# Kernel optimization log

Hardware: AMD Instinct MI355X
Metric: run time of the kernel (lower is better)

The kernel has to match this reference:

```python
import jax, jax.numpy as jnp
import numpy as np

B, T, P, V, D, DINO, H, L = 32, 40, 256, 4096, 256, 384, 4, 2
HD = D // H          # head dim 64
DFF = 4 * D          # 1024
EPS = 1e-5


def setup_inputs() -> dict:
    key = jax.random.key(0)
    ks = iter(jax.random.split(key, 40))
    rn = lambda shape, s=0.02: jax.random.normal(next(ks), shape, jnp.float32) * s
    return dict(
        patches=jax.random.normal(next(ks), (B, P, DINO), jnp.float32),
        tokens=jax.random.randint(next(ks), (B, T), 0, V, jnp.int32),
        tok_emb=rn((V, D)),
        pos_emb=rn((1, T, D)),
        qkv_w=rn((L, 3 * D, D)), qkv_b=jnp.zeros((L, 3 * D), jnp.float32),
        out_w=rn((L, D, D)), out_b=jnp.zeros((L, D), jnp.float32),
        ln1_s=jnp.ones((L, D), jnp.float32), ln1_b=jnp.zeros((L, D), jnp.float32),
        w1=rn((L, DFF, D)), b1=jnp.zeros((L, DFF), jnp.float32),
        w2=rn((L, D, DFF)), b2=jnp.zeros((L, D), jnp.float32),
        ln2_s=jnp.ones((L, D), jnp.float32), ln2_b=jnp.zeros((L, D), jnp.float32),
        fus_w1=rn((D, DINO + D)), fus_b1=jnp.zeros((D,), jnp.float32),
        fus_w2=rn((D, D)), fus_b2=jnp.zeros((D,), jnp.float32),
        cls_w=rn((V, D)), cls_b=jnp.zeros((V,), jnp.float32),
    )


def _ln(x, s, b):
    m = jnp.mean(x, -1, keepdims=True)
    v = jnp.var(x, -1, keepdims=True)
    return (x - m) * jax.lax.rsqrt(v + EPS) * s + b


def _token_encoder(tokens, tok_emb, pos_emb, qkv_w, qkv_b, out_w, out_b,
                   ln1_s, ln1_b, w1, b1, w2, b2, ln2_s, ln2_b):
    # Causal full-sequence pass: output at position t equals re-running the
    # unmasked encoder on tokens[:, :t+1] and taking the last position.
    x = tok_emb[tokens] + pos_emb[:, :tokens.shape[1], :]   # [B,T,D]
    causal = jnp.triu(jnp.full((T, T), -1e9, jnp.float32), 1)  # [T,T]
    for l in range(L):  # fixed small layer count
        qkv = x @ qkv_w[l].T + qkv_b[l]                     # [B,T,3D]
        q, k, v = jnp.split(qkv, 3, axis=-1)
        q = q.reshape(B, T, H, HD).transpose(0, 2, 1, 3)    # [B,H,T,hd]
        k = k.reshape(B, T, H, HD).transpose(0, 2, 1, 3)
        v = v.reshape(B, T, H, HD).transpose(0, 2, 1, 3)
        scores = jnp.einsum('bhqd,bhkd->bhqk', q, k) / np.sqrt(HD).astype(np.float32)
        attn = jax.nn.softmax(scores + causal, axis=-1)
        ctx = jnp.einsum('bhqk,bhkd->bhqd', attn, v)        # [B,H,T,hd]
        ctx = ctx.transpose(0, 2, 1, 3).reshape(B, T, D)
        x = _ln(x + ctx @ out_w[l].T + out_b[l], ln1_s[l], ln1_b[l])
        h = jax.nn.relu(x @ w1[l].T + b1[l]) @ w2[l].T + b2[l]
        x = _ln(x + h, ln2_s[l], ln2_b[l])
    return x  # [B,T,D]


def reference(patches, tokens, tok_emb, pos_emb, qkv_w, qkv_b, out_w, out_b,
              ln1_s, ln1_b, w1, b1, w2, b2, ln2_s, ln2_b,
              fus_w1, fus_b1, fus_w2, fus_b2, cls_w, cls_b):
    enc = _token_encoder(tokens, tok_emb, pos_emb, qkv_w, qkv_b, out_w, out_b,
                         ln1_s, ln1_b, w1, b1, w2, b2, ln2_s, ln2_b)  # [B,T,D]
    # context for step 0 is zeros; step t>0 uses encoder output at position t-1
    ctx = jnp.concatenate([jnp.zeros((B, 1, D), enc.dtype), enc[:, :-1]], axis=1)  # [B,T,D]
    # fusion MLP: split the concat-linear into a patch part and a context part
    wp, wc = fus_w1[:, :DINO], fus_w1[:, DINO:]
    pproj = patches @ wp.T                                  # [B,P,D]
    cproj = ctx @ wc.T + fus_b1                             # [B,T,D]
    h = jax.nn.gelu(pproj[:, None, :, :] + cproj[:, :, None, :], approximate=False)  # [B,T,P,D]
    fused = h @ fus_w2.T + fus_b2                           # [B,T,P,D]
    # sigmoid+gather of the 4096-way logits == gather classifier rows, dot, sigmoid
    w_sel = cls_w[tokens]                                   # [B,T,D]
    b_sel = cls_b[tokens]                                   # [B,T]
    logits = jnp.einsum('btpd,btd->btp', fused, w_sel) + b_sel[:, :, None]
    probs = jax.nn.sigmoid(logits)                          # [B,T,P]
    return probs.transpose(0, 2, 1)                         # [B,P,T] == [B,256,40]
```

## Files before the change

kernel.cpp:

```cpp
#include <hip/hip_runtime.h>
#include <hip/hip_bf16.h>

#define B_ 32
#define T_ 40
#define P_ 256
#define V_ 4096
#define D_ 256
#define DINO_ 384
#define H_ 4
#define L_ 2
#define HD_ 64
#define DFF_ 1024
#define EPS_ 1e-5f

typedef __bf16 bf16;
typedef __bf16 bf16x8 __attribute__((ext_vector_type(8)));
typedef float f32x4 __attribute__((ext_vector_type(4)));

#define OFF_QKV 0
#define OFF_OUTW 393216
#define OFF_W1 524288
#define OFF_W2 1048576
#define OFF_FUS 1572864
#define WB_TOTAL 1736704
#define CONV_BLOCKS 848

__device__ __forceinline__ bf16x8 cvt8(const float* p) {
  float4 f0 = *(const float4*)p;
  float4 f1 = *(const float4*)(p + 4);
  bf16x8 v;
  v[0] = (bf16)f0.x; v[1] = (bf16)f0.y; v[2] = (bf16)f0.z; v[3] = (bf16)f0.w;
  v[4] = (bf16)f1.x; v[5] = (bf16)f1.y; v[6] = (bf16)f1.z; v[7] = (bf16)f1.w;
  return v;
}

__global__ __launch_bounds__(256) void prep_k(
    const int* __restrict__ tokens, const float* __restrict__ tok_emb,
    const float* __restrict__ pos_emb, float* __restrict__ x,
    const float* __restrict__ fus_w2, bf16* __restrict__ w2Tb,
    const float* __restrict__ qkv_w, const float* __restrict__ out_w,
    const float* __restrict__ w1, const float* __restrict__ w2,
    const float* __restrict__ fus_w1, bf16* __restrict__ wb) {
  __shared__ float tile[32][33];
  int bi = blockIdx.x;
  int tid = threadIdx.x;
  if (bi < B_ * T_) {
    int t = bi % T_;
    x[bi * D_ + tid] = tok_emb[tokens[bi] * D_ + tid] + pos_emb[t * D_ + tid];
  } else if (bi < B_ * T_ + 64) {
    int tt = bi - B_ * T_;
    int bx = (tt & 7) * 32, by = (tt >> 3) * 32;
    int tx = tid & 31, ty = tid >> 5;
#pragma unroll
    for (int i = 0; i < 32; i += 8) tile[ty + i][tx] = fus_w2[(by + ty + i) * D_ + bx + tx];
    __syncthreads();
#pragma unroll
    for (int i = 0; i < 32; i += 8)
      w2Tb[(bx + ty + i) * D_ + by + tx] = (bf16)tile[tx][ty + i];
  } else {
    long f = (long)(bi - B_ * T_ - 64) * 2048 + tid * 8;
    const float* src;
    long off;
    if (f < OFF_OUTW)      { src = qkv_w;  off = f - OFF_QKV; }
    else if (f < OFF_W1)   { src = out_w;  off = f - OFF_OUTW; }
    else if (f < OFF_W2)   { src = w1;     off = f - OFF_W1; }
    else if (f < OFF_FUS)  { src = w2;     off = f - OFF_W2; }
    else                   { src = fus_w1; off = f - OFF_FUS; }
    *(bf16x8*)&wb[f] = cvt8(src + off);
  }
}

__global__ __launch_bounds__(256) void gemm_k(
    const float* __restrict__ A, const bf16* __restrict__ W,
    const float* __restrict__ bias, float* __restrict__ out,
    int K, int lda, int ldw, int ldc, int relu) {
  __shared__ bf16 As[32 * 72];
  __shared__ bf16 Ws[32 * 72];
  const int tid = threadIdx.x;
  const int lane = tid & 63;
  const int wv = tid >> 6;
  const int mi = wv & 1, ni = wv >> 1;
  const int col = lane & 15;
  const int quad = lane >> 4;
  const int bn = blockIdx.x * 32;
  const int bm = blockIdx.y * 32;
  const int srow = tid >> 3;
  const int kc = (tid & 7) * 8;
  const float* Ap = A + (long)(bm + srow) * lda;
  const bf16* Wp = W + (long)(bn + srow) * ldw;

  f32x4 acc = {0.f, 0.f, 0.f, 0.f};
  for (int kk = 0; kk < K; kk += 64) {
    *(bf16x8*)&As[srow * 72 + kc] = cvt8(Ap + kk + kc);
    *(bf16x8*)&Ws[srow * 72 + kc] = *(const bf16x8*)(Wp + kk + kc);
    __syncthreads();
#pragma unroll
    for (int ki = 0; ki < 2; ++ki) {
      bf16x8 afr = *(const bf16x8*)&As[(mi * 16 + col) * 72 + ki * 32 + quad * 8];
      bf16x8 bfr = *(const bf16x8*)&Ws[(ni * 16 + col) * 72 + ki * 32 + quad * 8];
      acc = __builtin_amdgcn_mfma_f32_16x16x32_bf16(afr, bfr, acc, 0, 0, 0);
    }
    __syncthreads();
  }
  const int n = bn + ni * 16 + col;
  float bv = bias ? bias[n] : 0.0f;
#pragma unroll
  for (int r = 0; r < 4; ++r) {
    int m = bm + mi * 16 + quad * 4 + r;
    float val = acc[r] + bv;
    if (relu) val = fmaxf(val, 0.0f);
    out[(long)m * ldc + n] = val;
  }
}

__global__ __launch_bounds__(256) void fuse3_k(
    const float* __restrict__ patches, const float* __restrict__ xbuf,
    const float* __restrict__ cls_w, const bf16* __restrict__ fusb,
    const bf16* __restrict__ w2Tb, const float* __restrict__ fus_b1,
    const int* __restrict__ tokens, float* __restrict__ pprojT,
    float* __restrict__ cw) {
  __shared__ bf16 As[32 * 72];
  __shared__ bf16 Ws[32 * 72];
  const int tid = threadIdx.x;
  const int lane = tid & 63;
  const int wv = tid >> 6;
  const int mi = wv & 1, ni = wv >> 1;
  const int col = lane & 15;
  const int quad = lane >> 4;
  const int bn = blockIdx.x * 32;
  const int y = blockIdx.y;
  const int srow = tid >> 3;
  const int kc = (tid & 7) * 8;

  int job, bm;
  if (y < 256) { job = 0; bm = y * 32; }
  else if (y < 296) { job = 1; bm = (y - 256) * 32; }
  else { job = 2; bm = (y - 296) * 32; }
  const int gm = bm + srow;

  const float* Ap;
  const bf16* Wp;
  int K;
  bool zeroA = false;
  if (job == 0) {
    Ap = patches + (long)gm * DINO_;
    Wp = fusb + (long)(bn + srow) * 640;
    K = DINO_;
  } else if (job == 1) {
    int t = gm % T_;
    zeroA = (t == 0);
    Ap = xbuf + (long)(zeroA ? gm : gm - 1) * D_;
    Wp = fusb + 384 + (long)(bn + srow) * 640;
    K = D_;
  } else {
    Ap = cls_w + (long)tokens[gm] * D_;
    Wp = w2Tb + (long)(bn + srow) * D_;
    K = D_;
  }

  f32x4 acc = {0.f, 0.f, 0.f, 0.f};
  bf16x8 z8 = {};
  for (int kk = 0; kk < K; kk += 64) {
    bf16x8 av = zeroA ? z8 : cvt8(Ap + kk + kc);
    *(bf16x8*)&As[srow * 72 + kc] = av;
    *(bf16x8*)&Ws[srow * 72 + kc] = *(const bf16x8*)(Wp + kk + kc);
    __syncthreads();
#pragma unroll
    for (int ki = 0; ki < 2; ++ki) {
      bf16x8 afr = *(const bf16x8*)&As[(mi * 16 + col) * 72 + ki * 32 + quad * 8];
      bf16x8 bfr = *(const bf16x8*)&Ws[(ni * 16 + col) * 72 + ki * 32 + quad * 8];
      acc = __builtin_amdgcn_mfma_f32_16x16x32_bf16(afr, bfr, acc, 0, 0, 0);
    }
    __syncthreads();
  }
  const int n = bn + ni * 16 + col;
  if (job == 0) {
#pragma unroll
    for (int r = 0; r < 4; ++r) {
      int m = bm + mi * 16 + quad * 4 + r;
      int b = m >> 8, p = m & 255;
      pprojT[(long)b * (D_ * P_) + (long)n * P_ + p] = acc[r];
    }
  } else if (job == 1) {
    float bv = fus_b1[n];
#pragma unroll
    for (int r = 0; r < 4; ++r) {
      int m = bm + mi * 16 + quad * 4 + r;
      cw[(long)m * (2 * D_) + n * 2] = acc[r] + bv;
    }
  } else {
#pragma unroll
    for (int r = 0; r < 4; ++r) {
      int m = bm + mi * 16 + quad * 4 + r;
      cw[(long)m * (2 * D_) + n * 2 + 1] = acc[r];
    }
  }
}

__global__ __launch_bounds__(256) void attn_k(const float* __restrict__ qkv,
                                              float* __restrict__ ctx) {
  __shared__ float q[T_][HD_ + 1];
  __shared__ float k[T_][HD_ + 1];
  __shared__ float v[T_][HD_ + 1];
  __shared__ float s[T_][T_ + 1];
  int h = blockIdx.x, b = blockIdx.y;
  int tid = threadIdx.x;
  for (int idx = tid; idx < T_ * HD_; idx += 256) {
    int t = idx >> 6, d = idx & 63;
    long base = (long)(b * T_ + t) * (3 * D_) + h * HD_ + d;
    q[t][d] = qkv[base];
    k[t][d] = qkv[base + D_];
    v[t][d] = qkv[base + 2 * D_];
  }
  __syncthreads();
  for (int idx = tid; idx < T_ * T_; idx += 256) {
    int i = idx / T_, j = idx - i * T_;
    if (j <= i) {
      float acc = 0.f;
#pragma unroll
      for (int d = 0; d < HD_; ++d) acc += q[i][d] * k[j][d];
      s[i][j] = acc * 0.125f;
    }
  }
  __syncthreads();
  if (tid < T_) {
    int i = tid;
    float mx = -1e30f;
    for (int j = 0; j <= i; ++j) mx = fmaxf(mx, s[i][j]);
    float sum = 0.f;
    for (int j = 0; j <= i; ++j) {
      float e = __expf(s[i][j] - mx);
      s[i][j] = e;
      sum += e;
    }
    float inv = 1.0f / sum;
    for (int j = 0; j <= i; ++j) s[i][j] *= inv;
  }
  __syncthreads();
  for (int idx = tid; idx < T_ * HD_; idx += 256) {
    int i = idx >> 6, d = idx & 63;
    float acc = 0.f;
    for (int j = 0; j <= i; ++j) acc += s[i][j] * v[j][d];
    ctx[(long)(b * T_ + i) * D_ + h * HD_ + d] = acc;
  }
}

__global__ __launch_bounds__(256) void ln_k(float* __restrict__ x, const float* __restrict__ y,
                                            const float* __restrict__ g,
                                            const float* __restrict__ be) {
  __shared__ float red[4];
  int m = blockIdx.x, d = threadIdx.x;
  int lane = d & 63, wv = d >> 6;
  float val = x[m * D_ + d] + y[m * D_ + d];
  float sv = val;
#pragma unroll
  for (int mk = 1; mk < 64; mk <<= 1) sv += __shfl_xor(sv, mk);
  if (lane == 0) red[wv] = sv;
  __syncthreads();
  float mean = (red[0] + red[1] + red[2] + red[3]) * (1.0f / D_);
  __syncthreads();
  float c = val - mean;
  float s2 = c * c;
#pragma unroll
  for (int mk = 1; mk < 64; mk <<= 1) s2 += __shfl_xor(s2, mk);
  if (lane == 0) red[wv] = s2;
  __syncthreads();
  float var = (red[0] + red[1] + red[2] + red[3]) * (1.0f / D_);
  x[m * D_ + d] = c * rsqrtf(var + EPS_) * g[d] + be[d];
}

__global__ __launch_bounds__(256) void final_k(const float* __restrict__ pprojT,
                                               const float* __restrict__ cw,
                                               const int* __restrict__ tokens,
                                               const float* __restrict__ cls_w,
                                               const float* __restrict__ cls_b,
                                               const float* __restrict__ fus_b2,
                                               float* __restrict__ out) {
  int lane = threadIdx.x & 63, wv = threadIdx.x >> 6;
  int p = blockIdx.x * 64 + lane;
  int t = blockIdx.y * 4 + wv;
  int b = blockIdx.z;
  int m = b * T_ + t;
  int tok = tokens[m];
  const float* cr = cls_w + (long)tok * D_;
  float bacc = 0.f;
#pragma unroll
  for (int i = 0; i < 4; ++i) bacc += cr[lane + i * 64] * fus_b2[lane + i * 64];
#pragma unroll
  for (int mk = 1; mk < 64; mk <<= 1) bacc += __shfl_xor(bacc, mk);
  float beff = bacc + cls_b[tok];

  const float* ppb = pprojT + (long)b * (D_ * P_);
  const float* cwt = cw + (long)m * (D_ * 2);
  float acc = 0.f;
#pragma unroll 8
  for (int e = 0; e < D_; ++e) {
    float pp = ppb[e * P_ + p];
    float2 c = *(const float2*)&cwt[e * 2];
    float x = pp + c.x;
    float x2 = x * x;
    float u = x * fmaf(-0.1029432f, x2, -2.3022083f);
    float ex = __builtin_amdgcn_exp2f(u);
    float r = __builtin_amdgcn_rcpf(1.0f + ex);
    acc = fmaf(x * r, c.y, acc);
  }
  float logit = acc + beff;
  float es = __builtin_amdgcn_exp2f(-1.4426950408889634f * logit);
  out[(long)(b * P_ + p) * T_ + t] = __builtin_amdgcn_rcpf(1.0f + es);
}

extern "C" void kernel_launch(void* const* d_in, const int* in_sizes, int n_in, void* d_out,
                              int out_size, void* d_ws, size_t ws_size, hipStream_t stream) {
  const float* patches = (const float*)d_in[0];
  const int* tokens = (const int*)d_in[1];
  const float* tok_emb = (const float*)d_in[2];
  const float* pos_emb = (const float*)d_in[3];
  const float* qkv_w = (const float*)d_in[4];
  const float* qkv_b = (const float*)d_in[5];
  const float* out_w = (const float*)d_in[6];
  const float* out_b = (const float*)d_in[7];
  const float* ln1_s = (const float*)d_in[8];
  const float* ln1_b = (const float*)d_in[9];
  const float* w1 = (const float*)d_in[10];
  const float* b1 = (const float*)d_in[11];
  const float* w2 = (const float*)d_in[12];
  const float* b2 = (const float*)d_in[13];
  const float* ln2_s = (const float*)d_in[14];
  const float* ln2_b = (const float*)d_in[15];
  const float* fus_w1 = (const float*)d_in[16];
  const float* fus_b1 = (const float*)d_in[17];
  const float* fus_w2 = (const float*)d_in[18];
  const float* fus_b2 = (const float*)d_in[19];
  const float* cls_w = (const float*)d_in[20];
  const float* cls_b = (const float*)d_in[21];
  float* out = (float*)d_out;

  float* xbuf = (float*)d_ws;
  float* qkvbuf = xbuf + B_ * T_ * D_;
  float* tmp = qkvbuf + B_ * T_ * 3 * D_;
  float* hbuf = tmp + B_ * T_ * D_;
  float* pprojT = hbuf + B_ * T_ * DFF_;
  float* cwbuf = pprojT + (long)B_ * D_ * P_;
  bf16* wb = (bf16*)(cwbuf + B_ * T_ * D_ * 2);
  bf16* w2Tb = wb + WB_TOTAL;

  const int MT = B_ * T_;

  prep_k<<<MT + 64 + CONV_BLOCKS, 256, 0, stream>>>(
      tokens, tok_emb, pos_emb, xbuf, fus_w2, w2Tb, qkv_w, out_w, w1, w2, fus_w1, wb);

  for (int l = 0; l < L_; ++l) {
    gemm_k<<<dim3(24, 40), 256, 0, stream>>>(
        xbuf, wb + OFF_QKV + (long)l * 3 * D_ * D_, qkv_b + l * 3 * D_, qkvbuf,
        D_, D_, D_, 3 * D_, 0);
    attn_k<<<dim3(H_, B_), 256, 0, stream>>>(qkvbuf, hbuf);
    gemm_k<<<dim3(8, 40), 256, 0, stream>>>(
        hbuf, wb + OFF_OUTW + (long)l * D_ * D_, out_b + l * D_, tmp,
        D_, D_, D_, D_, 0);
    ln_k<<<MT, D_, 0, stream>>>(xbuf, tmp, ln1_s + l * D_, ln1_b + l * D_);
    gemm_k<<<dim3(32, 40), 256, 0, stream>>>(
        xbuf, wb + OFF_W1 + (long)l * DFF_ * D_, b1 + l * DFF_, hbuf,
        D_, D_, D_, DFF_, 1);
    gemm_k<<<dim3(8, 40), 256, 0, stream>>>(
        hbuf, wb + OFF_W2 + (long)l * D_ * DFF_, b2 + l * D_, tmp,
        DFF_, DFF_, DFF_, D_, 0);
    ln_k<<<MT, D_, 0, stream>>>(xbuf, tmp, ln2_s + l * D_, ln2_b + l * D_);
  }

  fuse3_k<<<dim3(8, 336), 256, 0, stream>>>(patches, xbuf, cls_w, wb + OFF_FUS, w2Tb,
                                            fus_b1, tokens, pprojT, cwbuf);

  final_k<<<dim3(4, 10, 32), 256, 0, stream>>>(pprojT, cwbuf, tokens, cls_w, cls_b,
                                               fus_b2, out);
}
```

Measured before the change: 269.8 us.

## Fuse residual into GEMMs, bf16 FFN hidden, split attention, LDS-cache final context

```diff
diff --git a/kernel.cpp b/kernel.cpp
--- a/kernel.cpp
+++ b/kernel.cpp
@@ -24,6 +24,7 @@
 #define OFF_FUS 1572864
 #define WB_TOTAL 1736704
 #define CONV_BLOCKS 848
+#define PAT_BLOCKS 1536
 
 __device__ __forceinline__ bf16x8 cvt8(const float* p) {
   float4 f0 = *(const float4*)p;
@@ -40,7 +41,8 @@
     const float* __restrict__ fus_w2, bf16* __restrict__ w2Tb,
     const float* __restrict__ qkv_w, const float* __restrict__ out_w,
     const float* __restrict__ w1, const float* __restrict__ w2,
-    const float* __restrict__ fus_w1, bf16* __restrict__ wb) {
+    const float* __restrict__ fus_w1, bf16* __restrict__ wb,
+    const float* __restrict__ patches, bf16* __restrict__ patb) {
   __shared__ float tile[32][33];
   int bi = blockIdx.x;
   int tid = threadIdx.x;
@@ -57,7 +59,7 @@
 #pragma unroll
     for (int i = 0; i < 32; i += 8)
       w2Tb[(bx + ty + i) * D_ + by + tx] = (bf16)tile[tx][ty + i];
-  } else {
+  } else if (bi < B_ * T_ + 64 + CONV_BLOCKS) {
     long f = (long)(bi - B_ * T_ - 64) * 2048 + tid * 8;
     const float* src;
     long off;
@@ -67,32 +69,37 @@
     else if (f < OFF_FUS)  { src = w2;     off = f - OFF_W2; }
     else                   { src = fus_w1; off = f - OFF_FUS; }
     *(bf16x8*)&wb[f] = cvt8(src + off);
-  }
-}
-
+  } else {
+    long f = (long)(bi - B_ * T_ - 64 - CONV_BLOCKS) * 2048 + tid * 8;
+    *(bf16x8*)&patb[f] = cvt8(patches + f);
+  }
+}
+
+template <int ABF16, int OBF16, int RELU, int RESID>
 __global__ __launch_bounds__(256) void gemm_k(
-    const float* __restrict__ A, const bf16* __restrict__ W,
-    const float* __restrict__ bias, float* __restrict__ out,
-    int K, int lda, int ldw, int ldc, int relu) {
+    const void* __restrict__ Av, const bf16* __restrict__ W,
+    const float* __restrict__ bias, const float* __restrict__ resid,
+    void* __restrict__ outv, int K, int lda, int ldw, int ldc) {
   __shared__ bf16 As[32 * 72];
   __shared__ bf16 Ws[32 * 72];
   const int tid = threadIdx.x;
   const int lane = tid & 63;
   const int wv = tid >> 6;
   const int mi = wv & 1, ni = wv >> 1;
-  const int col = lane & 15;
-  const int quad = lane >> 4;
-  const int bn = blockIdx.x * 32;
-  const int bm = blockIdx.y * 32;
-  const int srow = tid >> 3;
-  const int kc = (tid & 7) * 8;
-  const float* Ap = A + (long)(bm + srow) * lda;
-  const bf16* Wp = W + (long)(bn + srow) * ldw;
+  const int col = lane & 15, quad = lane >> 4;
+  const int bn = blockIdx.x * 32, bm = blockIdx.y * 32;
+  const int srow = tid >> 3, kc = (tid & 7) * 8;
+  const float* Af = (const float*)Av;
+  const bf16* Ab = (const bf16*)Av;
+  const bf16* Wp = W + (long)(bn + srow) * ldw + kc;
 
   f32x4 acc = {0.f, 0.f, 0.f, 0.f};
   for (int kk = 0; kk < K; kk += 64) {
-    *(bf16x8*)&As[srow * 72 + kc] = cvt8(Ap + kk + kc);
-    *(bf16x8*)&Ws[srow * 72 + kc] = *(const bf16x8*)(Wp + kk + kc);
+    if (ABF16)
+      *(bf16x8*)&As[srow * 72 + kc] = *(const bf16x8*)(Ab + (long)(bm + srow) * lda + kk + kc);
+    else
+      *(bf16x8*)&As[srow * 72 + kc] = cvt8(Af + (long)(bm + srow) * lda + kk + kc);
+    *(bf16x8*)&Ws[srow * 72 + kc] = *(const bf16x8*)(Wp + kk);
     __syncthreads();
 #pragma unroll
     for (int ki = 0; ki < 2; ++ki) {
@@ -108,13 +115,91 @@
   for (int r = 0; r < 4; ++r) {
     int m = bm + mi * 16 + quad * 4 + r;
     float val = acc[r] + bv;
-    if (relu) val = fmaxf(val, 0.0f);
-    out[(long)m * ldc + n] = val;
+    if (RESID) val += resid[(long)m * D_ + n];
+    if (RELU) val = fmaxf(val, 0.0f);
+    if (OBF16) ((bf16*)outv)[(long)m * ldc + n] = (bf16)val;
+    else ((float*)outv)[(long)m * ldc + n] = val;
+  }
+}
+
+__global__ __launch_bounds__(256) void ln_k(const float* __restrict__ s,
+                                            float* __restrict__ xout,
+                                            const float* __restrict__ g,
+                                            const float* __restrict__ be) {
+  int wv = threadIdx.x >> 6, lane = threadIdx.x & 63;
+  int m = blockIdx.x * 4 + wv;
+  float4 v = *(const float4*)(s + (long)m * D_ + lane * 4);
+  float sum = v.x + v.y + v.z + v.w;
+  float ss = v.x * v.x + v.y * v.y + v.z * v.z + v.w * v.w;
+#pragma unroll
+  for (int mk = 1; mk < 64; mk <<= 1) {
+    sum += __shfl_xor(sum, mk);
+    ss += __shfl_xor(ss, mk);
+  }
+  float mean = sum * (1.0f / D_);
+  float inv = rsqrtf(ss * (1.0f / D_) - mean * mean + EPS_);
+  float4 g4 = *(const float4*)(g + lane * 4);
+  float4 b4 = *(const float4*)(be + lane * 4);
+  float4 o;
+  o.x = (v.x - mean) * inv * g4.x + b4.x;
+  o.y = (v.y - mean) * inv * g4.y + b4.y;
+  o.z = (v.z - mean) * inv * g4.z + b4.z;
+  o.w = (v.w - mean) * inv * g4.w + b4.w;
+  *(float4*)(xout + (long)m * D_ + lane * 4) = o;
+}
+
+__global__ __launch_bounds__(256) void attn_k(const float* __restrict__ qkv,
+                                              float* __restrict__ ctx) {
+  __shared__ float q[20][HD_ + 1];
+  __shared__ float k[T_][HD_ + 1];
+  __shared__ float v[T_][HD_ + 1];
+  __shared__ float s[20][T_ + 1];
+  int h = blockIdx.x, b = blockIdx.y, zq = blockIdx.z;
+  int r0 = zq * 20;
+  int tid = threadIdx.x;
+  for (int idx = tid; idx < T_ * HD_; idx += 256) {
+    int t = idx >> 6, d = idx & 63;
+    long base = (long)(b * T_ + t) * (3 * D_) + h * HD_ + d;
+    k[t][d] = qkv[base + D_];
+    v[t][d] = qkv[base + 2 * D_];
+    if (t < 20) q[t][d] = qkv[(long)(b * T_ + r0 + t) * (3 * D_) + h * HD_ + d];
+  }
+  __syncthreads();
+  for (int idx = tid; idx < 20 * T_; idx += 256) {
+    int i = idx / T_, j = idx - i * T_;
+    if (j <= r0 + i) {
+      float acc = 0.f;
+#pragma unroll
+      for (int d = 0; d < HD_; ++d) acc += q[i][d] * k[j][d];
+      s[i][j] = acc * 0.125f;
+    }
+  }
+  __syncthreads();
+  if (tid < 20) {
+    int i = tid, hi = r0 + i;
+    float mx = -1e30f;
+    for (int j = 0; j <= hi; ++j) mx = fmaxf(mx, s[i][j]);
+    float sum = 0.f;
+    for (int j = 0; j <= hi; ++j) {
+      float e = __expf(s[i][j] - mx);
+      s[i][j] = e;
+      sum += e;
+    }
+    float inv = 1.0f / sum;
+    for (int j = 0; j <= hi; ++j) s[i][j] *= inv;
+  }
+  __syncthreads();
+  for (int idx = tid; idx < 20 * HD_; idx += 256) {
+    int i = idx >> 6, d = idx & 63;
+    int hi = r0 + i;
+    float acc = 0.f;
+    for (int j = 0; j <= hi; ++j) acc += s[i][j] * v[j][d];
+    ctx[(long)(b * T_ + hi) * D_ + h * HD_ + d] = acc;
   }
 }
 
 __global__ __launch_bounds__(256) void fuse3_k(
-    const float* __restrict__ patches, const float* __restrict__ xbuf,
+    const bf16* __restrict__ patb, const float* __restrict__ xbuf,
     const float* __restrict__ cls_w, const bf16* __restrict__ fusb,
     const bf16* __restrict__ w2Tb, const float* __restrict__ fus_b1,
     const int* __restrict__ tokens, float* __restrict__ pprojT,
@@ -125,12 +210,10 @@
   const int lane = tid & 63;
   const int wv = tid >> 6;
   const int mi = wv & 1, ni = wv >> 1;
-  const int col = lane & 15;
-  const int quad = lane >> 4;
+  const int col = lane & 15, quad = lane >> 4;
   const int bn = blockIdx.x * 32;
   const int y = blockIdx.y;
-  const int srow = tid >> 3;
-  const int kc = (tid & 7) * 8;
+  const int srow = tid >> 3, kc = (tid & 7) * 8;
 
   int job, bm;
   if (y < 256) { job = 0; bm = y * 32; }
@@ -138,32 +221,34 @@
   else { job = 2; bm = (y - 296) * 32; }
   const int gm = bm + srow;
 
-  const float* Ap;
   const bf16* Wp;
-  int K;
+  int K = D_;
   bool zeroA = false;
+  const float* Apf = nullptr;
+  const bf16* Apb = nullptr;
   if (job == 0) {
-    Ap = patches + (long)gm * DINO_;
-    Wp = fusb + (long)(bn + srow) * 640;
+    Apb = patb + (long)gm * DINO_;
+    Wp = fusb + (long)(bn + srow) * 640 + kc;
     K = DINO_;
   } else if (job == 1) {
     int t = gm % T_;
     zeroA = (t == 0);
-    Ap = xbuf + (long)(zeroA ? gm : gm - 1) * D_;
-    Wp = fusb + 384 + (long)(bn + srow) * 640;
-    K = D_;
+    Apf = xbuf + (long)(zeroA ? gm : gm - 1) * D_;
+    Wp = fusb + 384 + (long)(bn + srow) * 640 + kc;
   } else {
-    Ap = cls_w + (long)tokens[gm] * D_;
-    Wp = w2Tb + (long)(bn + srow) * D_;
-    K = D_;
+    Apf = cls_w + (long)tokens[gm] * D_;
+    Wp = w2Tb + (long)(bn + srow) * D_ + kc;
   }
 
   f32x4 acc = {0.f, 0.f, 0.f, 0.f};
   bf16x8 z8 = {};
   for (int kk = 0; kk < K; kk += 64) {
-    bf16x8 av = zeroA ? z8 : cvt8(Ap + kk + kc);
+    bf16x8 av;
+    if (job == 0) av = *(const bf16x8*)(Apb + kk + kc);
+    else if (zeroA) av = z8;
+    else av = cvt8(Apf + kk + kc);
     *(bf16x8*)&As[srow * 72 + kc] = av;
-    *(bf16x8*)&Ws[srow * 72 + kc] = *(const bf16x8*)(Wp + kk + kc);
+    *(bf16x8*)&Ws[srow * 72 + kc] = *(const bf16x8*)(Wp + kk);
     __syncthreads();
 #pragma unroll
     for (int ki = 0; ki < 2; ++ki) {
@@ -176,97 +261,25 @@
   const int n = bn + ni * 16 + col;
   if (job == 0) {
 #pragma unroll
-    for (int r = 0; r < 4; ++r) {
-      int m = bm + mi * 16 + quad * 4 + r;
+    for (int r4 = 0; r4 < 4; ++r4) {
+      int m = bm + mi * 16 + quad * 4 + r4;
       int b = m >> 8, p = m & 255;
-      pprojT[(long)b * (D_ * P_) + (long)n * P_ + p] = acc[r];
+      pprojT[(long)b * (D_ * P_) + (long)n * P_ + p] = acc[r4];
     }
   } else if (job == 1) {
     float bv = fus_b1[n];
 #pragma unroll
-    for (int r = 0; r < 4; ++r) {
-      int m = bm + mi * 16 + quad * 4 + r;
-      cw[(long)m * (2 * D_) + n * 2] = acc[r] + bv;
+    for (int r4 = 0; r4 < 4; ++r4) {
+      int m = bm + mi * 16 + quad * 4 + r4;
+      cw[(long)m * (2 * D_) + n * 2] = acc[r4] + bv;
     }
   } else {
 #pragma unroll
-    for (int r = 0; r < 4; ++r) {
-      int m = bm + mi * 16 + quad * 4 + r;
-      cw[(long)m * (2 * D_) + n * 2 + 1] = acc[r];
-    }
-  }
-}
-
-__global__ __launch_bounds__(256) void attn_k(const float* __restrict__ qkv,
-                                              float* __restrict__ ctx) {
-  __shared__ float q[T_][HD_ + 1];
-  __shared__ float k[T_][HD_ + 1];
-  __shared__ float v[T_][HD_ + 1];
-  __shared__ float s[T_][T_ + 1];
-  int h = blockIdx.x, b = blockIdx.y;
-  int tid = threadIdx.x;
-  for (int idx = tid; idx < T_ * HD_; idx += 256) {
-    int t = idx >> 6, d = idx & 63;
-    long base = (long)(b * T_ + t) * (3 * D_) + h * HD_ + d;
-    q[t][d] = qkv[base];
-    k[t][d] = qkv[base + D_];
-    v[t][d] = qkv[base + 2 * D_];
-  }
-  __syncthreads();
-  for (int idx = tid; idx < T_ * T_; idx += 256) {
-    int i = idx / T_, j = idx - i * T_;
-    if (j <= i) {
-      float acc = 0.f;
-#pragma unroll
-      for (int d = 0; d < HD_; ++d) acc += q[i][d] * k[j][d];
-      s[i][j] = acc * 0.125f;
-    }
-  }
-  __syncthreads();
-  if (tid < T_) {
-    int i = tid;
-    float mx = -1e30f;
-    for (int j = 0; j <= i; ++j) mx = fmaxf(mx, s[i][j]);
-    float sum = 0.f;
-    for (int j = 0; j <= i; ++j) {
-      float e = __expf(s[i][j] - mx);
-      s[i][j] = e;
-      sum += e;
-    }
-    float inv = 1.0f / sum;
-    for (int j = 0; j <= i; ++j) s[i][j] *= inv;
-  }
-  __syncthreads();
-  for (int idx = tid; idx < T_ * HD_; idx += 256) {
-    int i = idx >> 6, d = idx & 63;
-    float acc = 0.f;
-    for (int j = 0; j <= i; ++j) acc += s[i][j] * v[j][d];
-    ctx[(long)(b * T_ + i) * D_ + h * HD_ + d] = acc;
-  }
-}
-
-__global__ __launch_bounds__(256) void ln_k(float* __restrict__ x, const float* __restrict__ y,
-                                            const float* __restrict__ g,
-                                            const float* __restrict__ be) {
-  __shared__ float red[4];
-  int m = blockIdx.x, d = threadIdx.x;
-  int lane = d & 63, wv = d >> 6;
-  float val = x[m * D_ + d] + y[m * D_ + d];
-  float sv = val;
-#pragma unroll
-  for (int mk = 1; mk < 64; mk <<= 1) sv += __shfl_xor(sv, mk);
-  if (lane == 0) red[wv] = sv;
-  __syncthreads();
-  float mean = (red[0] + red[1] + red[2] + red[3]) * (1.0f / D_);
-  __syncthreads();
-  float c = val - mean;
-  float s2 = c * c;
-#pragma unroll
-  for (int mk = 1; mk < 64; mk <<= 1) s2 += __shfl_xor(s2, mk);
-  if (lane == 0) red[wv] = s2;
-  __syncthreads();
-  float var = (red[0] + red[1] + red[2] + red[3]) * (1.0f / D_);
-  x[m * D_ + d] = c * rsqrtf(var + EPS_) * g[d] + be[d];
+    for (int r4 = 0; r4 < 4; ++r4) {
+      int m = bm + mi * 16 + quad * 4 + r4;
+      cw[(long)m * (2 * D_) + n * 2 + 1] = acc[r4];
+    }
+  }
 }
 
 __global__ __launch_bounds__(256) void final_k(const float* __restrict__ pprojT,
@@ -276,10 +289,19 @@
                                                const float* __restrict__ cls_b,
                                                const float* __restrict__ fus_b2,
                                                float* __restrict__ out) {
-  int lane = threadIdx.x & 63, wv = threadIdx.x >> 6;
+  __shared__ float2 cws[4][D_];
+  int tid = threadIdx.x;
+  int lane = tid & 63, wv = tid >> 6;
   int p = blockIdx.x * 64 + lane;
   int t = blockIdx.y * 4 + wv;
   int b = blockIdx.z;
+  int mbase = b * T_ + blockIdx.y * 4;
+  for (int idx = tid; idx < 4 * D_; idx += 256) {
+    int tt = idx >> 8, e = idx & 255;
+    cws[tt][e] = ((const float2*)cw)[(long)(mbase + tt) * D_ + e];
+  }
+  __syncthreads();
+
   int m = b * T_ + t;
   int tok = tokens[m];
   const float* cr = cls_w + (long)tok * D_;
@@ -291,12 +313,11 @@
   float beff = bacc + cls_b[tok];
 
   const float* ppb = pprojT + (long)b * (D_ * P_);
-  const float* cwt = cw + (long)m * (D_ * 2);
   float acc = 0.f;
 #pragma unroll 8
   for (int e = 0; e < D_; ++e) {
     float pp = ppb[e * P_ + p];
-    float2 c = *(const float2*)&cwt[e * 2];
+    float2 c = cws[wv][e];
     float x = pp + c.x;
     float x2 = x * x;
     float u = x * fmaf(-0.1029432f, x2, -2.3022083f);
@@ -335,39 +356,38 @@
   const float* cls_b = (const float*)d_in[21];
   float* out = (float*)d_out;
 
-  float* xbuf = (float*)d_ws;
-  float* qkvbuf = xbuf + B_ * T_ * D_;
-  float* tmp = qkvbuf + B_ * T_ * 3 * D_;
-  float* hbuf = tmp + B_ * T_ * D_;
-  float* pprojT = hbuf + B_ * T_ * DFF_;
+  const int MT = B_ * T_;
+  float* x = (float*)d_ws;
+  float* qkvbuf = x + MT * D_;
+  float* attbuf = qkvbuf + MT * 3 * D_;
+  float* s = attbuf + MT * D_;
+  float* pprojT = s + MT * D_;
   float* cwbuf = pprojT + (long)B_ * D_ * P_;
-  bf16* wb = (bf16*)(cwbuf + B_ * T_ * D_ * 2);
+  bf16* wb = (bf16*)(cwbuf + MT * D_ * 2);
   bf16* w2Tb = wb + WB_TOTAL;
-
-  const int MT = B_ * T_;
-
-  prep_k<<<MT + 64 + CONV_BLOCKS, 256, 0, stream>>>(
-      tokens, tok_emb, pos_emb, xbuf, fus_w2, w2Tb, qkv_w, out_w, w1, w2, fus_w1, wb);
+  bf16* patb = w2Tb + D_ * D_;
+  bf16* hb = patb + (long)B_ * P_ * DINO_;
+
+  prep_k<<<MT + 64 + CONV_BLOCKS + PAT_BLOCKS, 256, 0, stream>>>(
+      tokens, tok_emb, pos_emb, x, fus_w2, w2Tb, qkv_w, out_w, w1, w2, fus_w1, wb,
+      patches, patb);
 
   for (int l = 0; l < L_; ++l) {
-    gemm_k<<<dim3(24, 40), 256, 0, stream>>>(
-        xbuf, wb + OFF_QKV + (long)l * 3 * D_ * D_, qkv_b + l * 3 * D_, qkvbuf,
-        D_, D_, D_, 3 * D_, 0);
-    attn_k<<<dim3(H_, B_), 256, 0, stream>>>(qkvbuf, hbuf);
-    gemm_k<<<dim3(8, 40), 256, 0, stream>>>(
-        hbuf, wb + OFF_OUTW + (long)l * D_ * D_, out_b + l * D_, tmp,
-        D_, D_, D_, D_, 0);
-    ln_k<<<MT, D_, 0, stream>>>(xbuf, tmp, ln1_s + l * D_, ln1_b + l * D_);
-    gemm_k<<<dim3(32, 40), 256, 0, stream>>>(
-        xbuf, wb + OFF_W1 + (long)l * DFF_ * D_, b1 + l * DFF_, hbuf,
-        D_, D_, D_, DFF_, 1);
-    gemm_k<<<dim3(8, 40), 256, 0, stream>>>(
-        hbuf, wb + OFF_W2 + (long)l * D_ * DFF_, b2 + l * D_, tmp,
-        DFF_, DFF_, DFF_, D_, 0);
-    ln_k<<<MT, D_, 0, stream>>>(xbuf, tmp, ln2_s + l * D_, ln2_b + l * D_);
-  }
-
-  fuse3_k<<<dim3(8, 336), 256, 0, stream>>>(patches, xbuf, cls_w, wb + OFF_FUS, w2Tb,
+    gemm_k<0, 0, 0, 0><<<dim3(24, 40), 256, 0, stream>>>(
+        x, wb + OFF_QKV + (long)l * 3 * D_ * D_, qkv_b + l * 3 * D_, nullptr, qkvbuf,
+        D_, D_, D_, 3 * D_);
+    attn_k<<<dim3(H_, B_, 2), 256, 0, stream>>>(qkvbuf, attbuf);
+    gemm_k<0, 0, 0, 1><<<dim3(8, 40), 256, 0, stream>>>(
+        attbuf, wb + OFF_OUTW + (long)l * D_ * D_, out_b + l * D_, x, s, D_, D_, D_, D_);
+    ln_k<<<MT / 4, 256, 0, stream>>>(s, x, ln1_s + l * D_, ln1_b + l * D_);
+    gemm_k<0, 1, 1, 0><<<dim3(32, 40), 256, 0, stream>>>(
+        x, wb + OFF_W1 + (long)l * DFF_ * D_, b1 + l * DFF_, nullptr, hb, D_, D_, D_, DFF_);
+    gemm_k<1, 0, 0, 1><<<dim3(8, 40), 256, 0, stream>>>(
+        hb, wb + OFF_W2 + (long)l * D_ * DFF_, b2 + l * D_, x, s, DFF_, DFF_, DFF_, D_);
+    ln_k<<<MT / 4, 256, 0, stream>>>(s, x, ln2_s + l * D_, ln2_b + l * D_);
+  }
+
+  fuse3_k<<<dim3(8, 336), 256, 0, stream>>>(patb, x, cls_w, wb + OFF_FUS, w2Tb,
                                             fus_b1, tokens, pprojT, cwbuf);
 
   final_k<<<dim3(4, 10, 32), 256, 0, stream>>>(pprojT, cwbuf, tokens, cls_w, cls_b,
```

Result: faster. 257.5 us (-4.6%).
